# Kernel tuning notes

Measured on AMD Instinct MI355X. Metric: run time of the kernel, lower is better.

## Reference

```python
import jax, jax.numpy as jnp
import numpy as np

NEG_SLOPE = 0.2  # PyG GATConv default leaky_relu slope


def gat_conv(x, src, dst, n, W, a_src, a_dst, bias, concat):
    """PyG-style GATConv (add_self_loops already applied to src/dst)."""
    H, C = a_src.shape
    h = (x @ W).reshape(n, H, C)                      # [N,H,C]
    al_src = jnp.einsum('nhc,hc->nh', h, a_src)       # [N,H]
    al_dst = jnp.einsum('nhc,hc->nh', h, a_dst)       # [N,H]
    e = jax.nn.leaky_relu(al_src[src] + al_dst[dst], NEG_SLOPE)  # [E,H]
    # segment softmax over incoming edges of each dst node
    m = jax.ops.segment_max(e, dst, num_segments=n)   # [N,H]
    ex = jnp.exp(e - m[dst])
    denom = jax.ops.segment_sum(ex, dst, num_segments=n)
    alpha = ex / denom[dst]                            # [E,H]
    out = jax.ops.segment_sum(h[src] * alpha[:, :, None], dst, num_segments=n)  # [N,H,C]
    if concat:
        out = out.reshape(n, H * C)
    else:
        out = out.mean(axis=1)
    return out + bias


def setup_inputs() -> dict:
    key = jax.random.key(0)
    ks = jax.random.split(key, 12)
    N, E = 100000, 1600000
    IN, HID, OUT, H = 128, 16, 32, 4
    x = jax.random.normal(ks[0], (N, IN), dtype=jnp.float32)
    edge_index = jax.random.randint(ks[1], (2, E), 0, N, dtype=jnp.int64)
    s = 0.1
    W1 = jax.random.normal(ks[2], (IN, H * HID), dtype=jnp.float32) * s
    a_src1 = jax.random.normal(ks[3], (H, HID), dtype=jnp.float32) * s
    a_dst1 = jax.random.normal(ks[4], (H, HID), dtype=jnp.float32) * s
    b1 = jnp.zeros((H * HID,), dtype=jnp.float32)
    W2 = jax.random.normal(ks[5], (H * HID, H * OUT), dtype=jnp.float32) * s
    a_src2 = jax.random.normal(ks[6], (H, OUT), dtype=jnp.float32) * s
    a_dst2 = jax.random.normal(ks[7], (H, OUT), dtype=jnp.float32) * s
    b2 = jnp.zeros((OUT,), dtype=jnp.float32)
    return {"x": x, "edge_index": edge_index,
            "W1": W1, "a_src1": a_src1, "a_dst1": a_dst1, "b1": b1,
            "W2": W2, "a_src2": a_src2, "a_dst2": a_dst2, "b2": b2}


def reference(x, edge_index, W1, a_src1, a_dst1, b1, W2, a_src2, a_dst2, b2):
    n = x.shape[0]
    loop = jnp.arange(n, dtype=edge_index.dtype)
    src = jnp.concatenate([edge_index[0], loop])
    dst = jnp.concatenate([edge_index[1], loop])
    # dropout is identity at inference
    h = gat_conv(x, src, dst, n, W1, a_src1, a_dst1, b1, concat=True)
    h = gat_conv(h, src, dst, n, W2, a_src2, a_dst2, b2, concat=False)
    h = jax.nn.elu(h)
    return jax.nn.log_softmax(h, axis=1)
```

## Files before the change

### kernel.cpp

```cpp
#include <hip/hip_runtime.h>
#include <hip/hip_fp16.h>
#include <cstdint>
#include <cstddef>

#define NEG 0.2f
#define TILE 4096
#define WEXP(e) __expf((e) > 0.f ? (e) : NEG * (e))

typedef _Float16 fh2 __attribute__((ext_vector_type(2)));

__device__ __forceinline__ fh2 bfh2(unsigned v) { fh2 r; *(unsigned*)&r = v; return r; }
__device__ __forceinline__ __half2 bch(int v) { __half2 r; *(int*)&r = v; return r; }

#if __has_builtin(__builtin_amdgcn_fdot2)
#define FDOT2(a, b, c) __builtin_amdgcn_fdot2((a), (b), (c), false)
#else
__device__ __forceinline__ float FDOT2(fh2 a, fh2 b, float c) {
    return fmaf((float)a.x, (float)b.x, fmaf((float)a.y, (float)b.y, c));
}
#endif


__global__ __launch_bounds__(256) void bhist_k(const int* __restrict__ ei, int* __restrict__ bc, int E, int nbk) {
    __shared__ int sb[256];
    int t = threadIdx.x;
    sb[t] = 0;
    __syncthreads();
    int stride = gridDim.x * 256;
    for (int i = blockIdx.x * 256 + t; i < E; i += stride) {
        int d = __builtin_nontemporal_load(ei + E + i);
        atomicAdd(&sb[d >> 9], 1);
    }
    __syncthreads();
    if (t < nbk && sb[t] > 0) atomicAdd(&bc[t], sb[t]);
}


__global__ __launch_bounds__(256) void bscan_k(const int* __restrict__ bc, int* __restrict__ bb,
                                               int* __restrict__ curA, int nbk) {
    __shared__ int sm[256];
    int t = threadIdx.x;
    int v = (t < nbk) ? bc[t] : 0;
    sm[t] = v; __syncthreads();
    for (int off = 1; off < 256; off <<= 1) {
        int u = (t >= off) ? sm[t - off] : 0;
        __syncthreads();
        sm[t] += u;
        __syncthreads();
    }
    if (t < nbk) {
        int ex = sm[t] - v;
        bb[t] = ex;
        curA[t] = ex;
        if (t == nbk - 1) bb[nbk] = sm[t];
    }
}


__global__ __launch_bounds__(256) void partA_k(const int* __restrict__ ei, int* __restrict__ curA,
                                               uint2* __restrict__ pairs, int E, int nbk) {
    __shared__ int scnt[256];
    __shared__ int sc[256];
    __shared__ int sbase[256];
    __shared__ int gbase[256];
    __shared__ int cur2[256];
    __shared__ int ssrc[TILE];
    __shared__ int sdst[TILE];
    int t = threadIdx.x;
    int ntiles = (E + TILE - 1) / TILE;
    for (int tile = blockIdx.x; tile < ntiles; tile += gridDim.x) {
        int base = tile * TILE;
        int cntE = min(TILE, E - base);
        scnt[t] = 0;
        __syncthreads();
        int mys[16], myd[16];
        #pragma unroll
        for (int j = 0; j < 16; j++) {
            int i = base + t + 256 * j;
            int s = 0, d = -1;
            if (i < E) {
                s = __builtin_nontemporal_load(ei + i);
                d = __builtin_nontemporal_load(ei + E + i);
            }
            mys[j] = s; myd[j] = d;
            if (d >= 0) atomicAdd(&scnt[d >> 9], 1);
        }
        __syncthreads();
        sc[t] = scnt[t];
        __syncthreads();
        for (int off = 1; off < 256; off <<= 1) {
            int u = (t >= off) ? sc[t - off] : 0;
            __syncthreads();
            sc[t] += u;
            __syncthreads();
        }
        int myb = sc[t] - scnt[t];
        sbase[t] = myb;
        cur2[t] = myb;
        if (t < nbk && scnt[t] > 0) gbase[t] = atomicAdd(&curA[t], scnt[t]);
        __syncthreads();
        #pragma unroll
        for (int j = 0; j < 16; j++) {
            int d = myd[j];
            if (d >= 0) {
                int b = d >> 9;
                int pos = atomicAdd(&cur2[b], 1);
                ssrc[pos] = mys[j];
                sdst[pos] = d;
            }
        }
        __syncthreads();
        for (int i = t; i < cntE; i += 256) {
            int d = sdst[i];
            int b = d >> 9;
            int addr = gbase[b] + (i - sbase[b]);
            pairs[addr] = make_uint2((unsigned)ssrc[i], (unsigned)d);
        }
        __syncthreads();
    }
}


__global__ __launch_bounds__(256) void partB2_k(const uint2* __restrict__ pin, const int* __restrict__ bb,
                                                int* __restrict__ rp, int* __restrict__ cnt,
                                                int* __restrict__ srcout, int N) {
    __shared__ int cur[512];
    __shared__ int sc[512];
    int b = blockIdx.x, t = threadIdx.x;
    int d0 = b << 9;
    cur[t] = 0; cur[t + 256] = 0;
    __syncthreads();
    int ebase = bb[b], eend = bb[b + 1];
    for (int j = ebase + t; j < eend; j += 256) {
        int d = (int)pin[j].y;
        atomicAdd(&cur[d - d0], 1);
    }
    __syncthreads();
    sc[t] = cur[t]; sc[t + 256] = cur[t + 256];
    __syncthreads();
    for (int off = 1; off <= 256; off <<= 1) {
        int a0 = (t >= off) ? sc[t - off] : 0;
        int a1 = sc[t + 256 - off];
        __syncthreads();
        sc[t] += a0; sc[t + 256] += a1;
        __syncthreads();
    }
    int base0 = ebase + sc[t] - cur[t];
    int base1 = ebase + sc[t + 256] - cur[t + 256];
    if (d0 + t < N)       { rp[d0 + t] = base0;       cnt[d0 + t] = cur[t]; }
    if (d0 + t + 256 < N) { rp[d0 + t + 256] = base1; cnt[d0 + t + 256] = cur[t + 256]; }
    cur[t] = base0; cur[t + 256] = base1;
    __syncthreads();
    for (int j = ebase + t; j < eend; j += 256) {
        uint2 p = pin[j];
        int d = (int)p.y;
        int pos = atomicAdd(&cur[d - d0], 1);
        srcout[pos] = (int)p.x;
    }
}


__global__ __launch_bounds__(256) void gemm1_k(const float* __restrict__ x, const float* __restrict__ W,
                                               const float* __restrict__ a_src, const float* __restrict__ a_dst,
                                               __half* __restrict__ h, float* __restrict__ alsrc,
                                               float* __restrict__ aldst, int N) {
    __shared__ float Bs[128 * 64];
    __shared__ float xs[64][68];
    int t = threadIdx.x;
    for (int i = t; i < 128 * 64 / 4; i += 256)
        ((float4*)Bs)[i] = ((const float4*)W)[i];
    int ct = t & 15, rt = t >> 4;
    int head = ct >> 2, cq = ct & 3;
    float asv[4], adv[4];
    #pragma unroll
    for (int j = 0; j < 4; j++) {
        asv[j] = a_src[head * 16 + 4 * cq + j];
        adv[j] = a_dst[head * 16 + 4 * cq + j];
    }
    int ntiles = (N + 63) >> 6;
    for (int tile = blockIdx.x; tile < ntiles; tile += gridDim.x) {
        int r0 = tile << 6;
        float acc[4][4];
        #pragma unroll
        for (int i = 0; i < 4; i++)
            #pragma unroll
            for (int j = 0; j < 4; j++) acc[i][j] = 0.f;
        for (int kc = 0; kc < 128; kc += 64) {
            __syncthreads();
            int srow = t >> 4, sf4 = t & 15;
            #pragma unroll
            for (int p = 0; p < 4; p++) {
                int r = r0 + srow + 16 * p;
                float4 v = make_float4(0.f, 0.f, 0.f, 0.f);
                if (r < N) v = *(const float4*)(x + (size_t)r * 128 + kc + 4 * sf4);
                *(float4*)&xs[srow + 16 * p][4 * sf4] = v;
            }
            __syncthreads();
            #pragma unroll 4
            for (int k = 0; k < 64; k++) {
                float4 bv = *(float4*)&Bs[(kc + k) * 64 + 4 * ct];
                #pragma unroll
                for (int i = 0; i < 4; i++) {
                    float xv = xs[4 * rt + i][k];
                    acc[i][0] = fmaf(xv, bv.x, acc[i][0]);
                    acc[i][1] = fmaf(xv, bv.y, acc[i][1]);
                    acc[i][2] = fmaf(xv, bv.z, acc[i][2]);
                    acc[i][3] = fmaf(xv, bv.w, acc[i][3]);
                }
            }
        }
        #pragma unroll
        for (int i = 0; i < 4; i++) {
            int r = r0 + 4 * rt + i;
            float ps = 0.f, pd = 0.f;
            #pragma unroll
            for (int j = 0; j < 4; j++) {
                ps = fmaf(acc[i][j], asv[j], ps);
                pd = fmaf(acc[i][j], adv[j], pd);
            }
            ps += __shfl_xor(ps, 1); ps += __shfl_xor(ps, 2);
            pd += __shfl_xor(pd, 1); pd += __shfl_xor(pd, 2);
            if (r < N) {
                __half2 h0 = __floats2half2_rn(acc[i][0], acc[i][1]);
                __half2 h1 = __floats2half2_rn(acc[i][2], acc[i][3]);
                *(__half2*)(h + (size_t)r * 64 + 4 * ct) = h0;
                *(__half2*)(h + (size_t)r * 64 + 4 * ct + 2) = h1;
                if (cq == 0) { alsrc[r * 4 + head] = ps; aldst[r * 4 + head] = pd; }
            }
        }
    }
}


__global__ __launch_bounds__(256) void node1_k(const __half* __restrict__ h, const int* __restrict__ srccol,
                                               const float* __restrict__ alsrc, const float* __restrict__ aldst,
                                               const int* __restrict__ rp, const int* __restrict__ cnt,
                                               const float* __restrict__ bias, __half* __restrict__ out, int N) {
    int t = threadIdx.x;
    int d = (blockIdx.x * 256 + t) >> 4;
    if (d >= N) return;
    int c = t & 15;
    int hc = c >> 2;
    const __half2* hb = (const __half2*)h;
    unsigned co = 2u * c;
    float ad = aldst[d * 4 + hc];
    float e = alsrc[d * 4 + hc] + ad;
    float w = WEXP(e);
    float den = w;
    __half2 wp = __float2half2_rn(w);
    uint2 u = *(const uint2*)(hb + ((unsigned)d << 5) + co);
    __half2 acc0 = __hmul2(wp, *(__half2*)&u.x);
    __half2 acc1 = __hmul2(wp, *(__half2*)&u.y);
    int start = rp[d], deg = cnt[d];
    int i = 0;
    for (; i + 3 < deg; i += 4) {
        int s0 = srccol[start + i];
        int s1 = srccol[start + i + 1];
        int s2 = srccol[start + i + 2];
        int s3 = srccol[start + i + 3];
        uint2 u0 = *(const uint2*)(hb + ((unsigned)s0 << 5) + co);
        uint2 u1 = *(const uint2*)(hb + ((unsigned)s1 << 5) + co);
        uint2 u2 = *(const uint2*)(hb + ((unsigned)s2 << 5) + co);
        uint2 u3 = *(const uint2*)(hb + ((unsigned)s3 << 5) + co);
        float e0 = alsrc[s0 * 4 + hc] + ad;
        float e1 = alsrc[s1 * 4 + hc] + ad;
        float e2 = alsrc[s2 * 4 + hc] + ad;
        float e3 = alsrc[s3 * 4 + hc] + ad;
        float w0 = WEXP(e0);
        float w1 = WEXP(e1);
        float w2 = WEXP(e2);
        float w3 = WEXP(e3);
        den += (w0 + w1) + (w2 + w3);
        __half2 p0 = __float2half2_rn(w0), p1 = __float2half2_rn(w1);
        __half2 p2 = __float2half2_rn(w2), p3 = __float2half2_rn(w3);
        acc0 = __hfma2(p0, *(__half2*)&u0.x, acc0);
        acc1 = __hfma2(p0, *(__half2*)&u0.y, acc1);
        acc0 = __hfma2(p1, *(__half2*)&u1.x, acc0);
        acc1 = __hfma2(p1, *(__half2*)&u1.y, acc1);
        acc0 = __hfma2(p2, *(__half2*)&u2.x, acc0);
        acc1 = __hfma2(p2, *(__half2*)&u2.y, acc1);
        acc0 = __hfma2(p3, *(__half2*)&u3.x, acc0);
        acc1 = __hfma2(p3, *(__half2*)&u3.y, acc1);
    }
    for (; i < deg; i++) {
        int s = srccol[start + i];
        uint2 us = *(const uint2*)(hb + ((unsigned)s << 5) + co);
        float es = alsrc[s * 4 + hc] + ad;
        float ws = WEXP(es);
        den += ws;
        __half2 wps = __float2half2_rn(ws);
        acc0 = __hfma2(wps, *(__half2*)&us.x, acc0);
        acc1 = __hfma2(wps, *(__half2*)&us.y, acc1);
    }
    float inv = 1.f / den;
    float2 f0 = __half22float2(acc0), f1 = __half22float2(acc1);
    float4 b = *(const float4*)(bias + 4 * c);
    __half2 o0 = __floats2half2_rn(f0.x * inv + b.x, f0.y * inv + b.y);
    __half2 o1 = __floats2half2_rn(f1.x * inv + b.z, f1.y * inv + b.w);
    uint2 o; o.x = *(unsigned*)&o0; o.y = *(unsigned*)&o1;
    *(uint2*)(out + (size_t)d * 64 + 4 * c) = o;
}


__global__ __launch_bounds__(256) void prew_k(const float* __restrict__ W2, const float* __restrict__ as2,
                                              const float* __restrict__ ad2, float* __restrict__ was,
                                              float* __restrict__ wad) {
    int t = threadIdx.x;
    int k = t >> 2, hh = t & 3;
    const float* wrow = W2 + k * 128 + hh * 32;
    const float* av = as2 + hh * 32;
    const float* dv = ad2 + hh * 32;
    float s = 0.f, ds = 0.f;
    #pragma unroll 8
    for (int c = 0; c < 32; c++) {
        float w = wrow[c];
        s = fmaf(w, av[c], s);
        ds = fmaf(w, dv[c], ds);
    }
    was[t] = s;
    wad[t] = ds;
}


__global__ __launch_bounds__(256) void alv2_k(const __half* __restrict__ h1o, const float* __restrict__ was,
                                              const float* __restrict__ wad, float* __restrict__ alsrc,
                                              float* __restrict__ aldst, int N) {
    int t = threadIdx.x;
    int d = (blockIdx.x * 256 + t) >> 4;
    if (d >= N) return;
    int c = t & 15;
    uint2 u = *(const uint2*)(h1o + (size_t)d * 64 + 4 * c);
    float2 f0 = __half22float2(*(__half2*)&u.x);
    float2 f1 = __half22float2(*(__half2*)&u.y);
    float v0 = f0.x, v1 = f0.y, v2 = f1.x, v3 = f1.y;
    const float4* was4 = (const float4*)was;
    const float4* wad4 = (const float4*)wad;
    float4 wa0 = was4[4 * c + 0], wa1 = was4[4 * c + 1], wa2 = was4[4 * c + 2], wa3 = was4[4 * c + 3];
    float4 wd0 = wad4[4 * c + 0], wd1 = wad4[4 * c + 1], wd2 = wad4[4 * c + 2], wd3 = wad4[4 * c + 3];
    float4 ps, pd;
    ps.x = fmaf(v0, wa0.x, fmaf(v1, wa1.x, fmaf(v2, wa2.x, v3 * wa3.x)));
    ps.y = fmaf(v0, wa0.y, fmaf(v1, wa1.y, fmaf(v2, wa2.y, v3 * wa3.y)));
    ps.z = fmaf(v0, wa0.z, fmaf(v1, wa1.z, fmaf(v2, wa2.z, v3 * wa3.z)));
    ps.w = fmaf(v0, wa0.w, fmaf(v1, wa1.w, fmaf(v2, wa2.w, v3 * wa3.w)));
    pd.x = fmaf(v0, wd0.x, fmaf(v1, wd1.x, fmaf(v2, wd2.x, v3 * wd3.x)));
    pd.y = fmaf(v0, wd0.y, fmaf(v1, wd1.y, fmaf(v2, wd2.y, v3 * wd3.y)));
    pd.z = fmaf(v0, wd0.z, fmaf(v1, wd1.z, fmaf(v2, wd2.z, v3 * wd3.z)));
    pd.w = fmaf(v0, wd0.w, fmaf(v1, wd1.w, fmaf(v2, wd2.w, v3 * wd3.w)));
    #pragma unroll
    for (int off = 1; off <= 8; off <<= 1) {
        ps.x += __shfl_xor(ps.x, off); ps.y += __shfl_xor(ps.y, off);
        ps.z += __shfl_xor(ps.z, off); ps.w += __shfl_xor(ps.w, off);
        pd.x += __shfl_xor(pd.x, off); pd.y += __shfl_xor(pd.y, off);
        pd.z += __shfl_xor(pd.z, off); pd.w += __shfl_xor(pd.w, off);
    }
    if (c == 0) {
        *(float4*)(alsrc + (size_t)d * 4) = ps;
        *(float4*)(aldst + (size_t)d * 4) = pd;
    }
}


#define EDGE_SH(J, U) { \
    __half2 l_ = *(__half2*)&U.x, h_ = *(__half2*)&U.y; \
    __half2 qa = bch(__shfl(wi, 4 * J + 0, 16)); \
    __half2 qb = bch(__shfl(wi, 4 * J + 1, 16)); \
    __half2 qc = bch(__shfl(wi, 4 * J + 2, 16)); \
    __half2 qd = bch(__shfl(wi, 4 * J + 3, 16)); \
    aA0 = __hfma2(qa, l_, aA0); aA1 = __hfma2(qa, h_, aA1); \
    aB0 = __hfma2(qb, l_, aB0); aB1 = __hfma2(qb, h_, aB1); \
    aC0 = __hfma2(qc, l_, aC0); aC1 = __hfma2(qc, h_, aC1); \
    aD0 = __hfma2(qd, l_, aD0); aD1 = __hfma2(qd, h_, aD1); }

__global__ __launch_bounds__(256) void node2_k(const __half* __restrict__ h1o, const int* __restrict__ srccol,
                                               const float* __restrict__ alsrc, const float* __restrict__ aldst,
                                               const int* __restrict__ rp, const int* __restrict__ cnt,
                                               __half* __restrict__ y, int N) {
    int t = threadIdx.x;
    int d = (blockIdx.x * 256 + t) >> 4;
    if (d >= N) return;
    int c = t & 15;
    int eh = c >> 2;
    int hh = c & 3;
    const uint2* hb = (const uint2*)h1o;
    float myad = aldst[d * 4 + hh];
    float selfw = WEXP(alsrc[d * 4 + hh] + myad);
    __half2 selfh = __float2half2_rn(selfw);
    int selfi = *(int*)&selfh;
    float mden = (eh == 0) ? selfw : 0.f;
    uint2 u = hb[((size_t)d << 4) + c];
    __half2 lo = *(__half2*)&u.x, hi = *(__half2*)&u.y;
    __half2 sA = bch(__shfl(selfi, 0, 16));
    __half2 sB = bch(__shfl(selfi, 1, 16));
    __half2 sC = bch(__shfl(selfi, 2, 16));
    __half2 sD = bch(__shfl(selfi, 3, 16));
    __half2 aA0 = __hmul2(sA, lo), aA1 = __hmul2(sA, hi);
    __half2 aB0 = __hmul2(sB, lo), aB1 = __hmul2(sB, hi);
    __half2 aC0 = __hmul2(sC, lo), aC1 = __hmul2(sC, hi);
    __half2 aD0 = __hmul2(sD, lo), aD1 = __hmul2(sD, hi);
    int start = rp[d], deg = cnt[d];
    int i = 0;
    for (; i + 3 < deg; i += 4) {
        int s0 = srccol[start + i];
        int s1 = srccol[start + i + 1];
        int s2 = srccol[start + i + 2];
        int s3 = srccol[start + i + 3];
        uint2 u0 = hb[((size_t)s0 << 4) + c];
        uint2 u1 = hb[((size_t)s1 << 4) + c];
        uint2 u2 = hb[((size_t)s2 << 4) + c];
        uint2 u3 = hb[((size_t)s3 << 4) + c];
        int my = (eh == 0) ? s0 : (eh == 1) ? s1 : (eh == 2) ? s2 : s3;
        float w = WEXP(alsrc[my * 4 + hh] + myad);
        mden += w;
        __half2 wh = __float2half2_rn(w);
        int wi = *(int*)&wh;
        EDGE_SH(0, u0)
        EDGE_SH(1, u1)
        EDGE_SH(2, u2)
        EDGE_SH(3, u3)
    }
    for (; i < deg; i++) {
        int s = srccol[start + i];
        uint2 us = hb[((size_t)s << 4) + c];
        float w = WEXP(alsrc[s * 4 + hh] + myad);
        mden += (eh == 0) ? w : 0.f;
        __half2 wh = __float2half2_rn(w);
        int wi = *(int*)&wh;
        EDGE_SH(0, us)
    }
    mden += __shfl_xor(mden, 4, 16);
    mden += __shfl_xor(mden, 8, 16);
    float dnA = __shfl(mden, 0, 16);
    float dnB = __shfl(mden, 1, 16);
    float dnC = __shfl(mden, 2, 16);
    float dnD = __shfl(mden, 3, 16);
    __half2 jA = __float2half2_rn(0.25f / dnA), jB = __float2half2_rn(0.25f / dnB);
    __half2 jC = __float2half2_rn(0.25f / dnC), jD = __float2half2_rn(0.25f / dnD);
    uint2 oA, oB, oC, oD;
    ((__half2*)&oA)[0] = __hmul2(jA, aA0); ((__half2*)&oA)[1] = __hmul2(jA, aA1);
    ((__half2*)&oB)[0] = __hmul2(jB, aB0); ((__half2*)&oB)[1] = __hmul2(jB, aB1);
    ((__half2*)&oC)[0] = __hmul2(jC, aC0); ((__half2*)&oC)[1] = __hmul2(jC, aC1);
    ((__half2*)&oD)[0] = __hmul2(jD, aD0); ((__half2*)&oD)[1] = __hmul2(jD, aD1);
    __half* yp = y + (size_t)d * 256 + 4u * (unsigned)c;
    *(uint2*)(yp)       = oA;
    *(uint2*)(yp + 64)  = oB;
    *(uint2*)(yp + 128) = oC;
    *(uint2*)(yp + 192) = oD;
}


__global__ __launch_bounds__(256) void gemm3_k(const __half* __restrict__ y, const float* __restrict__ W2,
                                               const float* __restrict__ bias, float* __restrict__ out, int N) {
    __shared__ unsigned wk[128 * 32];
    __shared__ unsigned ys[64 * 130];
    int t = threadIdx.x;
    for (int i = t; i < 4096; i += 256) {
        int k2 = i >> 5, col = i & 31;
        int hh = k2 >> 5, kk = (2 * k2) & 63;
        float f0 = W2[kk * 128 + hh * 32 + col];
        float f1 = W2[(kk + 1) * 128 + hh * 32 + col];
        __half2 hv = __floats2half2_rn(f0, f1);
        wk[i] = *(unsigned*)&hv;
    }
    int ct = t & 7, rt = t >> 3;
    float4 b4 = *(const float4*)(bias + 4 * ct);
    int r0 = blockIdx.x << 6;
    for (int i = t; i < 64 * 64; i += 256) {
        int row = i >> 6, k4 = i & 63;
        uint2 v = make_uint2(0u, 0u);
        int r = r0 + row;
        if (r < N) v = *(const uint2*)(y + (size_t)r * 256 + 4 * k4);
        *(uint2*)&ys[row * 130 + 2 * k4] = v;
    }
    __syncthreads();
    float acc[2][4];
    #pragma unroll
    for (int r = 0; r < 2; r++)
        #pragma unroll
        for (int j = 0; j < 4; j++) acc[r][j] = 0.f;
    const unsigned* yr0 = ys + (2 * rt) * 130;
    const unsigned* yr1 = yr0 + 130;
    const unsigned* wp = wk + 4 * ct;
    #pragma unroll 8
    for (int k2 = 0; k2 < 128; k2++) {
        fh2 xa = bfh2(yr0[k2]);
        fh2 xb = bfh2(yr1[k2]);
        uint2 w01 = *(const uint2*)&wp[k2 * 32];
        uint2 w23 = *(const uint2*)&wp[k2 * 32 + 2];
        fh2 w0 = bfh2(w01.x), w1 = bfh2(w01.y), w2 = bfh2(w23.x), w3 = bfh2(w23.y);
        acc[0][0] = FDOT2(xa, w0, acc[0][0]);
        acc[0][1] = FDOT2(xa, w1, acc[0][1]);
        acc[0][2] = FDOT2(xa, w2, acc[0][2]);
        acc[0][3] = FDOT2(xa, w3, acc[0][3]);
        acc[1][0] = FDOT2(xb, w0, acc[1][0]);
        acc[1][1] = FDOT2(xb, w1, acc[1][1]);
        acc[1][2] = FDOT2(xb, w2, acc[1][2]);
        acc[1][3] = FDOT2(xb, w3, acc[1][3]);
    }
    #pragma unroll
    for (int r = 0; r < 2; r++) {
        int row = r0 + 2 * rt + r;
        float ev0 = acc[r][0] + b4.x;
        float ev1 = acc[r][1] + b4.y;
        float ev2 = acc[r][2] + b4.z;
        float ev3 = acc[r][3] + b4.w;
        ev0 = ev0 > 0.f ? ev0 : __expf(ev0) - 1.f;
        ev1 = ev1 > 0.f ? ev1 : __expf(ev1) - 1.f;
        ev2 = ev2 > 0.f ? ev2 : __expf(ev2) - 1.f;
        ev3 = ev3 > 0.f ? ev3 : __expf(ev3) - 1.f;
        float mx = fmaxf(fmaxf(ev0, ev1), fmaxf(ev2, ev3));
        #pragma unroll
        for (int off = 1; off <= 4; off <<= 1) mx = fmaxf(mx, __shfl_xor(mx, off));
        float sm = __expf(ev0 - mx) + __expf(ev1 - mx) + __expf(ev2 - mx) + __expf(ev3 - mx);
        #pragma unroll
        for (int off = 1; off <= 4; off <<= 1) sm += __shfl_xor(sm, off);
        float ls = mx + __logf(sm);
        if (row < N) {
            float4 o;
            o.x = ev0 - ls; o.y = ev1 - ls; o.z = ev2 - ls; o.w = ev3 - ls;
            *(float4*)(out + (size_t)row * 32 + 4 * ct) = o;
        }
    }
}


extern "C" void kernel_launch(void* const* d_in, const int* in_sizes, int n_in,
                              void* d_out, int out_size, void* d_ws, size_t ws_size,
                              hipStream_t stream) {
    const float* x   = (const float*)d_in[0];
    const int*   ei  = (const int*)d_in[1];
    const float* W1  = (const float*)d_in[2];
    const float* as1 = (const float*)d_in[3];
    const float* ad1 = (const float*)d_in[4];
    const float* b1  = (const float*)d_in[5];
    const float* W2  = (const float*)d_in[6];
    const float* as2 = (const float*)d_in[7];
    const float* ad2 = (const float*)d_in[8];
    const float* b2  = (const float*)d_in[9];
    float* out = (float*)d_out;
    int N = in_sizes[0] / 128;
    int E = in_sizes[1] / 2;

    char* base = (char*)d_ws;
    size_t off = 0;
    auto alloc = [&](size_t bytes) -> char* {
        char* p = base + off;
        off = (off + bytes + 255) & ~(size_t)255;
        return p;
    };
    __half* y     = (__half*)alloc((size_t)N * 256 * 2);
    __half* h1h   = (__half*)y;
    uint2*  pairs = (uint2*)((char*)y + (size_t)N * 64 * 2);
    __half* h1o   = (__half*)alloc((size_t)N * 64 * 2);
    float* alsrc1 = (float*)alloc((size_t)N * 4 * 4);
    float* aldst1 = (float*)alloc((size_t)N * 4 * 4);
    float* alsrc2 = (float*)alloc((size_t)N * 4 * 4);
    float* aldst2 = (float*)alloc((size_t)N * 4 * 4);
    float* was    = (float*)alloc(256 * 4);
    float* wad    = (float*)alloc(256 * 4);
    int* cnt  = (int*)alloc((size_t)N * 4);
    int* rp   = (int*)alloc((size_t)N * 4);
    int* curA = (int*)alloc(256 * 4);
    int* bc   = (int*)alloc(256 * 4);
    int* bb   = (int*)alloc(260 * 4);
    int* srccol = (int*)alloc((size_t)E * 4);

    int nbk = (N + 511) >> 9;
    int ntilesA = (E + TILE - 1) / TILE;
    int nt1 = (N + 63) >> 6;

    prew_k<<<1, 256, 0, stream>>>(W2, as2, ad2, was, wad);
    hipMemsetAsync(bc, 0, 256 * 4, stream);
    bhist_k<<<512, 256, 0, stream>>>(ei, bc, E, nbk);
    bscan_k<<<1, 256, 0, stream>>>(bc, bb, curA, nbk);
    partA_k<<<ntilesA, 256, 0, stream>>>(ei, curA, pairs, E, nbk);
    partB2_k<<<nbk, 256, 0, stream>>>(pairs, bb, rp, cnt, srccol, N);

    gemm1_k<<<(nt1 + 1) / 2, 256, 0, stream>>>(x, W1, as1, ad1, h1h, alsrc1, aldst1, N);
    node1_k<<<(N + 15) / 16, 256, 0, stream>>>(h1h, srccol, alsrc1, aldst1, rp, cnt, b1, h1o, N);
    alv2_k<<<(N + 15) / 16, 256, 0, stream>>>(h1o, was, wad, alsrc2, aldst2, N);
    node2_k<<<(N + 15) / 16, 256, 0, stream>>>(h1o, srccol, alsrc2, aldst2, rp, cnt, y, N);
    gemm3_k<<<nt1, 256, 0, stream>>>(y, W2, b2, out, N);
}
```

Measured before the change: 344.0 us.

## Fuse layer-2 attention logits into node1, prefetch edge gathers, retile gemm3

Merges the alv2 pass into node1, so layer-2 attention logits come from the freshly computed node output without a second kernel reading h1o. Both aggregation kernels now load source indices as 16-byte vectors. They also software-pipeline the gathers one quad ahead and share one attention exp per lane through shuffles. gemm3 moves to 32-row tiles with packed fp16 FMA accumulation flushed to fp32 every 16 k-steps, instead of fdot2 into fp32, which adds precision risk in exchange for throughput.

```diff
diff --git a/kernel.cpp b/kernel.cpp
--- a/kernel.cpp
+++ b/kernel.cpp
@@ -7,18 +7,15 @@
 #define TILE 4096
 #define WEXP(e) __expf((e) > 0.f ? (e) : NEG * (e))
 
-typedef _Float16 fh2 __attribute__((ext_vector_type(2)));
-
-__device__ __forceinline__ fh2 bfh2(unsigned v) { fh2 r; *(unsigned*)&r = v; return r; }
-__device__ __forceinline__ __half2 bch(int v) { __half2 r; *(int*)&r = v; return r; }
-
-#if __has_builtin(__builtin_amdgcn_fdot2)
-#define FDOT2(a, b, c) __builtin_amdgcn_fdot2((a), (b), (c), false)
-#else
-__device__ __forceinline__ float FDOT2(fh2 a, fh2 b, float c) {
-    return fmaf((float)a.x, (float)b.x, fmaf((float)a.y, (float)b.y, c));
-}
-#endif
+typedef int i4v __attribute__((ext_vector_type(4)));
+
+__device__ __forceinline__ i4v ld_i4(const int* p) {
+    i4v r;
+    __builtin_memcpy(&r, p, 16);
+    return r;
+}
+__device__ __forceinline__ __half2 bch(unsigned v) { __half2 r; *(unsigned*)&r = v; return r; }
+__device__ __forceinline__ __half2 bchi(int v) { __half2 r; *(int*)&r = v; return r; }
 
 
 __global__ __launch_bounds__(256) void bhist_k(const int* __restrict__ ei, int* __restrict__ bc, int E, int nbk) {
@@ -232,76 +229,6 @@
 }
 
 
-__global__ __launch_bounds__(256) void node1_k(const __half* __restrict__ h, const int* __restrict__ srccol,
-                                               const float* __restrict__ alsrc, const float* __restrict__ aldst,
-                                               const int* __restrict__ rp, const int* __restrict__ cnt,
-                                               const float* __restrict__ bias, __half* __restrict__ out, int N) {
-    int t = threadIdx.x;
-    int d = (blockIdx.x * 256 + t) >> 4;
-    if (d >= N) return;
-    int c = t & 15;
-    int hc = c >> 2;
-    const __half2* hb = (const __half2*)h;
-    unsigned co = 2u * c;
-    float ad = aldst[d * 4 + hc];
-    float e = alsrc[d * 4 + hc] + ad;
-    float w = WEXP(e);
-    float den = w;
-    __half2 wp = __float2half2_rn(w);
-    uint2 u = *(const uint2*)(hb + ((unsigned)d << 5) + co);
-    __half2 acc0 = __hmul2(wp, *(__half2*)&u.x);
-    __half2 acc1 = __hmul2(wp, *(__half2*)&u.y);
-    int start = rp[d], deg = cnt[d];
-    int i = 0;
-    for (; i + 3 < deg; i += 4) {
-        int s0 = srccol[start + i];
-        int s1 = srccol[start + i + 1];
-        int s2 = srccol[start + i + 2];
-        int s3 = srccol[start + i + 3];
-        uint2 u0 = *(const uint2*)(hb + ((unsigned)s0 << 5) + co);
-        uint2 u1 = *(const uint2*)(hb + ((unsigned)s1 << 5) + co);
-        uint2 u2 = *(const uint2*)(hb + ((unsigned)s2 << 5) + co);
-        uint2 u3 = *(const uint2*)(hb + ((unsigned)s3 << 5) + co);
-        float e0 = alsrc[s0 * 4 + hc] + ad;
-        float e1 = alsrc[s1 * 4 + hc] + ad;
-        float e2 = alsrc[s2 * 4 + hc] + ad;
-        float e3 = alsrc[s3 * 4 + hc] + ad;
-        float w0 = WEXP(e0);
-        float w1 = WEXP(e1);
-        float w2 = WEXP(e2);
-        float w3 = WEXP(e3);
-        den += (w0 + w1) + (w2 + w3);
-        __half2 p0 = __float2half2_rn(w0), p1 = __float2half2_rn(w1);
-        __half2 p2 = __float2half2_rn(w2), p3 = __float2half2_rn(w3);
-        acc0 = __hfma2(p0, *(__half2*)&u0.x, acc0);
-        acc1 = __hfma2(p0, *(__half2*)&u0.y, acc1);
-        acc0 = __hfma2(p1, *(__half2*)&u1.x, acc0);
-        acc1 = __hfma2(p1, *(__half2*)&u1.y, acc1);
-        acc0 = __hfma2(p2, *(__half2*)&u2.x, acc0);
-        acc1 = __hfma2(p2, *(__half2*)&u2.y, acc1);
-        acc0 = __hfma2(p3, *(__half2*)&u3.x, acc0);
-        acc1 = __hfma2(p3, *(__half2*)&u3.y, acc1);
-    }
-    for (; i < deg; i++) {
-        int s = srccol[start + i];
-        uint2 us = *(const uint2*)(hb + ((unsigned)s << 5) + co);
-        float es = alsrc[s * 4 + hc] + ad;
-        float ws = WEXP(es);
-        den += ws;
-        __half2 wps = __float2half2_rn(ws);
-        acc0 = __hfma2(wps, *(__half2*)&us.x, acc0);
-        acc1 = __hfma2(wps, *(__half2*)&us.y, acc1);
-    }
-    float inv = 1.f / den;
-    float2 f0 = __half22float2(acc0), f1 = __half22float2(acc1);
-    float4 b = *(const float4*)(bias + 4 * c);
-    __half2 o0 = __floats2half2_rn(f0.x * inv + b.x, f0.y * inv + b.y);
-    __half2 o1 = __floats2half2_rn(f1.x * inv + b.z, f1.y * inv + b.w);
-    uint2 o; o.x = *(unsigned*)&o0; o.y = *(unsigned*)&o1;
-    *(uint2*)(out + (size_t)d * 64 + 4 * c) = o;
-}
-
-
 __global__ __launch_bounds__(256) void prew_k(const float* __restrict__ W2, const float* __restrict__ as2,
                                               const float* __restrict__ ad2, float* __restrict__ was,
                                               float* __restrict__ wad) {
@@ -322,17 +249,91 @@
 }
 
 
-__global__ __launch_bounds__(256) void alv2_k(const __half* __restrict__ h1o, const float* __restrict__ was,
-                                              const float* __restrict__ wad, float* __restrict__ alsrc,
-                                              float* __restrict__ aldst, int N) {
+__global__ __launch_bounds__(256) void node1_k(const __half* __restrict__ h, const int* __restrict__ srccol,
+                                               const float* __restrict__ alsrc, const float* __restrict__ aldst,
+                                               const int* __restrict__ rp, const int* __restrict__ cnt,
+                                               const float* __restrict__ bias,
+                                               const float* __restrict__ was, const float* __restrict__ wad,
+                                               __half* __restrict__ out,
+                                               float* __restrict__ alsrc2, float* __restrict__ aldst2, int N) {
     int t = threadIdx.x;
     int d = (blockIdx.x * 256 + t) >> 4;
     if (d >= N) return;
     int c = t & 15;
-    uint2 u = *(const uint2*)(h1o + (size_t)d * 64 + 4 * c);
-    float2 f0 = __half22float2(*(__half2*)&u.x);
-    float2 f1 = __half22float2(*(__half2*)&u.y);
-    float v0 = f0.x, v1 = f0.y, v2 = f1.x, v3 = f1.y;
+    int eh = c >> 2, hh = c & 3;
+    int mh = c >> 2;
+    const uint2* hb = (const uint2*)h;
+    float myad = aldst[d * 4 + hh];
+    float selfw = WEXP(alsrc[d * 4 + hh] + myad);
+    __half2 sh2 = __float2half2_rn(selfw);
+    int si = *(int*)&sh2;
+    float mden = (eh == 0) ? selfw : 0.f;
+    uint2 u = hb[((size_t)d << 4) + c];
+    __half2 smy = bchi(__shfl(si, mh, 16));
+    __half2 acc0 = __hmul2(smy, bch(u.x));
+    __half2 acc1 = __hmul2(smy, bch(u.y));
+    int start = rp[d], deg = cnt[d];
+    int nq = deg >> 2;
+    int i = 0;
+    #define N1_PROC(G0, G1, G2, G3, AW) { \
+        float w_ = WEXP((AW) + myad); \
+        mden += w_; \
+        __half2 wh_ = __float2half2_rn(w_); \
+        int wi_ = *(int*)&wh_; \
+        __half2 q0_ = bchi(__shfl(wi_, 0 + mh, 16)); \
+        __half2 q1_ = bchi(__shfl(wi_, 4 + mh, 16)); \
+        __half2 q2_ = bchi(__shfl(wi_, 8 + mh, 16)); \
+        __half2 q3_ = bchi(__shfl(wi_, 12 + mh, 16)); \
+        acc0 = __hfma2(q0_, bch(G0.x), acc0); acc1 = __hfma2(q0_, bch(G0.y), acc1); \
+        acc0 = __hfma2(q1_, bch(G1.x), acc0); acc1 = __hfma2(q1_, bch(G1.y), acc1); \
+        acc0 = __hfma2(q2_, bch(G2.x), acc0); acc1 = __hfma2(q2_, bch(G2.y), acc1); \
+        acc0 = __hfma2(q3_, bch(G3.x), acc0); acc1 = __hfma2(q3_, bch(G3.y), acc1); }
+    if (nq > 0) {
+        i4v sv = ld_i4(srccol + start);
+        uint2 g0 = hb[((size_t)(unsigned)sv.x << 4) + c];
+        uint2 g1 = hb[((size_t)(unsigned)sv.y << 4) + c];
+        uint2 g2 = hb[((size_t)(unsigned)sv.z << 4) + c];
+        uint2 g3 = hb[((size_t)(unsigned)sv.w << 4) + c];
+        int my = (eh == 0) ? sv.x : (eh == 1) ? sv.y : (eh == 2) ? sv.z : sv.w;
+        float aw = alsrc[(size_t)my * 4 + hh];
+        i4v nv = (nq > 1) ? ld_i4(srccol + start + 4) : sv;
+        for (int q = 1; q < nq; q++) {
+            uint2 n0 = hb[((size_t)(unsigned)nv.x << 4) + c];
+            uint2 n1 = hb[((size_t)(unsigned)nv.y << 4) + c];
+            uint2 n2 = hb[((size_t)(unsigned)nv.z << 4) + c];
+            uint2 n3 = hb[((size_t)(unsigned)nv.w << 4) + c];
+            int nmy = (eh == 0) ? nv.x : (eh == 1) ? nv.y : (eh == 2) ? nv.z : nv.w;
+            float naw = alsrc[(size_t)nmy * 4 + hh];
+            i4v nv2 = (q + 1 < nq) ? ld_i4(srccol + start + 4 * (q + 1)) : nv;
+            N1_PROC(g0, g1, g2, g3, aw)
+            g0 = n0; g1 = n1; g2 = n2; g3 = n3; aw = naw; nv = nv2;
+        }
+        N1_PROC(g0, g1, g2, g3, aw)
+        i = nq << 2;
+    }
+    for (; i < deg; i++) {
+        int s = srccol[start + i];
+        uint2 us = hb[((size_t)(unsigned)s << 4) + c];
+        float w = WEXP(alsrc[(size_t)s * 4 + hh] + myad);
+        mden += (eh == 0) ? w : 0.f;
+        __half2 wh = __float2half2_rn(w);
+        int wi = *(int*)&wh;
+        __half2 qq = bchi(__shfl(wi, mh, 16));
+        acc0 = __hfma2(qq, bch(us.x), acc0);
+        acc1 = __hfma2(qq, bch(us.y), acc1);
+    }
+    mden += __shfl_xor(mden, 4, 16);
+    mden += __shfl_xor(mden, 8, 16);
+    float den = __shfl(mden, mh, 16);
+    float inv = 1.f / den;
+    float2 f0 = __half22float2(acc0), f1 = __half22float2(acc1);
+    float4 b = *(const float4*)(bias + 4 * c);
+    float v0 = f0.x * inv + b.x, v1 = f0.y * inv + b.y;
+    float v2 = f1.x * inv + b.z, v3 = f1.y * inv + b.w;
+    __half2 o0 = __floats2half2_rn(v0, v1);
+    __half2 o1 = __floats2half2_rn(v2, v3);
+    uint2 o; o.x = *(unsigned*)&o0; o.y = *(unsigned*)&o1;
+    *(uint2*)(out + (size_t)d * 64 + 4 * c) = o;
     const float4* was4 = (const float4*)was;
     const float4* wad4 = (const float4*)wad;
     float4 wa0 = was4[4 * c + 0], wa1 = was4[4 * c + 1], wa2 = was4[4 * c + 2], wa3 = was4[4 * c + 3];
@@ -354,18 +355,18 @@
         pd.z += __shfl_xor(pd.z, off); pd.w += __shfl_xor(pd.w, off);
     }
     if (c == 0) {
-        *(float4*)(alsrc + (size_t)d * 4) = ps;
-        *(float4*)(aldst + (size_t)d * 4) = pd;
+        *(float4*)(alsrc2 + (size_t)d * 4) = ps;
+        *(float4*)(aldst2 + (size_t)d * 4) = pd;
     }
 }
 
 
 #define EDGE_SH(J, U) { \
-    __half2 l_ = *(__half2*)&U.x, h_ = *(__half2*)&U.y; \
-    __half2 qa = bch(__shfl(wi, 4 * J + 0, 16)); \
-    __half2 qb = bch(__shfl(wi, 4 * J + 1, 16)); \
-    __half2 qc = bch(__shfl(wi, 4 * J + 2, 16)); \
-    __half2 qd = bch(__shfl(wi, 4 * J + 3, 16)); \
+    __half2 l_ = bch(U.x), h_ = bch(U.y); \
+    __half2 qa = bchi(__shfl(wi, 4 * J + 0, 16)); \
+    __half2 qb = bchi(__shfl(wi, 4 * J + 1, 16)); \
+    __half2 qc = bchi(__shfl(wi, 4 * J + 2, 16)); \
+    __half2 qd = bchi(__shfl(wi, 4 * J + 3, 16)); \
     aA0 = __hfma2(qa, l_, aA0); aA1 = __hfma2(qa, h_, aA1); \
     aB0 = __hfma2(qb, l_, aB0); aB1 = __hfma2(qb, h_, aB1); \
     aC0 = __hfma2(qc, l_, aC0); aC1 = __hfma2(qc, h_, aC1); \
@@ -388,40 +389,51 @@
     int selfi = *(int*)&selfh;
     float mden = (eh == 0) ? selfw : 0.f;
     uint2 u = hb[((size_t)d << 4) + c];
-    __half2 lo = *(__half2*)&u.x, hi = *(__half2*)&u.y;
-    __half2 sA = bch(__shfl(selfi, 0, 16));
-    __half2 sB = bch(__shfl(selfi, 1, 16));
-    __half2 sC = bch(__shfl(selfi, 2, 16));
-    __half2 sD = bch(__shfl(selfi, 3, 16));
+    __half2 lo = bch(u.x), hi = bch(u.y);
+    __half2 sA = bchi(__shfl(selfi, 0, 16));
+    __half2 sB = bchi(__shfl(selfi, 1, 16));
+    __half2 sC = bchi(__shfl(selfi, 2, 16));
+    __half2 sD = bchi(__shfl(selfi, 3, 16));
     __half2 aA0 = __hmul2(sA, lo), aA1 = __hmul2(sA, hi);
     __half2 aB0 = __hmul2(sB, lo), aB1 = __hmul2(sB, hi);
     __half2 aC0 = __hmul2(sC, lo), aC1 = __hmul2(sC, hi);
     __half2 aD0 = __hmul2(sD, lo), aD1 = __hmul2(sD, hi);
     int start = rp[d], deg = cnt[d];
+    int nq = deg >> 2;
     int i = 0;
-    for (; i + 3 < deg; i += 4) {
-        int s0 = srccol[start + i];
-        int s1 = srccol[start + i + 1];
-        int s2 = srccol[start + i + 2];
-        int s3 = srccol[start + i + 3];
-        uint2 u0 = hb[((size_t)s0 << 4) + c];
-        uint2 u1 = hb[((size_t)s1 << 4) + c];
-        uint2 u2 = hb[((size_t)s2 << 4) + c];
-        uint2 u3 = hb[((size_t)s3 << 4) + c];
-        int my = (eh == 0) ? s0 : (eh == 1) ? s1 : (eh == 2) ? s2 : s3;
-        float w = WEXP(alsrc[my * 4 + hh] + myad);
-        mden += w;
-        __half2 wh = __float2half2_rn(w);
-        int wi = *(int*)&wh;
-        EDGE_SH(0, u0)
-        EDGE_SH(1, u1)
-        EDGE_SH(2, u2)
-        EDGE_SH(3, u3)
+    #define N2_PROC(G0, G1, G2, G3, AW) { \
+        float w_ = WEXP((AW) + myad); \
+        mden += w_; \
+        __half2 wh_ = __float2half2_rn(w_); \
+        int wi = *(int*)&wh_; \
+        EDGE_SH(0, G0) EDGE_SH(1, G1) EDGE_SH(2, G2) EDGE_SH(3, G3) }
+    if (nq > 0) {
+        i4v sv = ld_i4(srccol + start);
+        uint2 g0 = hb[((size_t)(unsigned)sv.x << 4) + c];
+        uint2 g1 = hb[((size_t)(unsigned)sv.y << 4) + c];
+        uint2 g2 = hb[((size_t)(unsigned)sv.z << 4) + c];
+        uint2 g3 = hb[((size_t)(unsigned)sv.w << 4) + c];
+        int my = (eh == 0) ? sv.x : (eh == 1) ? sv.y : (eh == 2) ? sv.z : sv.w;
+        float aw = alsrc[(size_t)my * 4 + hh];
+        i4v nv = (nq > 1) ? ld_i4(srccol + start + 4) : sv;
+        for (int q = 1; q < nq; q++) {
+            uint2 n0 = hb[((size_t)(unsigned)nv.x << 4) + c];
+            uint2 n1 = hb[((size_t)(unsigned)nv.y << 4) + c];
+            uint2 n2 = hb[((size_t)(unsigned)nv.z << 4) + c];
+            uint2 n3 = hb[((size_t)(unsigned)nv.w << 4) + c];
+            int nmy = (eh == 0) ? nv.x : (eh == 1) ? nv.y : (eh == 2) ? nv.z : nv.w;
+            float naw = alsrc[(size_t)nmy * 4 + hh];
+            i4v nv2 = (q + 1 < nq) ? ld_i4(srccol + start + 4 * (q + 1)) : nv;
+            N2_PROC(g0, g1, g2, g3, aw)
+            g0 = n0; g1 = n1; g2 = n2; g3 = n3; aw = naw; nv = nv2;
+        }
+        N2_PROC(g0, g1, g2, g3, aw)
+        i = nq << 2;
     }
     for (; i < deg; i++) {
         int s = srccol[start + i];
-        uint2 us = hb[((size_t)s << 4) + c];
-        float w = WEXP(alsrc[s * 4 + hh] + myad);
+        uint2 us = hb[((size_t)(unsigned)s << 4) + c];
+        float w = WEXP(alsrc[(size_t)s * 4 + hh] + myad);
         mden += (eh == 0) ? w : 0.f;
         __half2 wh = __float2half2_rn(w);
         int wi = *(int*)&wh;
@@ -451,7 +463,7 @@
 __global__ __launch_bounds__(256) void gemm3_k(const __half* __restrict__ y, const float* __restrict__ W2,
                                                const float* __restrict__ bias, float* __restrict__ out, int N) {
     __shared__ unsigned wk[128 * 32];
-    __shared__ unsigned ys[64 * 130];
+    __shared__ unsigned ys[32 * 130];
     int t = threadIdx.x;
     for (int i = t; i < 4096; i += 256) {
         int k2 = i >> 5, col = i & 31;
@@ -463,8 +475,8 @@
     }
     int ct = t & 7, rt = t >> 3;
     float4 b4 = *(const float4*)(bias + 4 * ct);
-    int r0 = blockIdx.x << 6;
-    for (int i = t; i < 64 * 64; i += 256) {
+    int r0 = blockIdx.x << 5;
+    for (int i = t; i < 32 * 64; i += 256) {
         int row = i >> 6, k4 = i & 63;
         uint2 v = make_uint2(0u, 0u);
         int r = r0 + row;
@@ -472,53 +484,49 @@
         *(uint2*)&ys[row * 130 + 2 * k4] = v;
     }
     __syncthreads();
-    float acc[2][4];
+    float acc[4] = {0.f, 0.f, 0.f, 0.f};
+    const unsigned* yr = ys + rt * 130;
+    const unsigned* wp = wk + 4 * ct;
+    for (int kc = 0; kc < 128; kc += 16) {
+        __half2 h0 = __float2half2_rn(0.f), h1 = h0, h2 = h0, h3 = h0;
+        #pragma unroll
+        for (int j = 0; j < 16; j++) {
+            int k2 = kc + j;
+            __half2 x2 = bch(yr[k2]);
+            uint2 w01 = *(const uint2*)&wp[k2 * 32];
+            uint2 w23 = *(const uint2*)&wp[k2 * 32 + 2];
+            h0 = __hfma2(x2, bch(w01.x), h0);
+            h1 = __hfma2(x2, bch(w01.y), h1);
+            h2 = __hfma2(x2, bch(w23.x), h2);
+            h3 = __hfma2(x2, bch(w23.y), h3);
+        }
+        float2 q0 = __half22float2(h0), q1 = __half22float2(h1);
+        float2 q2 = __half22float2(h2), q3 = __half22float2(h3);
+        acc[0] += q0.x + q0.y;
+        acc[1] += q1.x + q1.y;
+        acc[2] += q2.x + q2.y;
+        acc[3] += q3.x + q3.y;
+    }
+    int row = r0 + rt;
+    float ev0 = acc[0] + b4.x;
+    float ev1 = acc[1] + b4.y;
+    float ev2 = acc[2] + b4.z;
+    float ev3 = acc[3] + b4.w;
+    ev0 = ev0 > 0.f ? ev0 : __expf(ev0) - 1.f;
+    ev1 = ev1 > 0.f ? ev1 : __expf(ev1) - 1.f;
+    ev2 = ev2 > 0.f ? ev2 : __expf(ev2) - 1.f;
+    ev3 = ev3 > 0.f ? ev3 : __expf(ev3) - 1.f;
+    float mx = fmaxf(fmaxf(ev0, ev1), fmaxf(ev2, ev3));
     #pragma unroll
-    for (int r = 0; r < 2; r++)
-        #pragma unroll
-        for (int j = 0; j < 4; j++) acc[r][j] = 0.f;
-    const unsigned* yr0 = ys + (2 * rt) * 130;
-    const unsigned* yr1 = yr0 + 130;
-    const unsigned* wp = wk + 4 * ct;
-    #pragma unroll 8
-    for (int k2 = 0; k2 < 128; k2++) {
-        fh2 xa = bfh2(yr0[k2]);
-        fh2 xb = bfh2(yr1[k2]);
-        uint2 w01 = *(const uint2*)&wp[k2 * 32];
-        uint2 w23 = *(const uint2*)&wp[k2 * 32 + 2];
-        fh2 w0 = bfh2(w01.x), w1 = bfh2(w01.y), w2 = bfh2(w23.x), w3 = bfh2(w23.y);
-        acc[0][0] = FDOT2(xa, w0, acc[0][0]);
-        acc[0][1] = FDOT2(xa, w1, acc[0][1]);
-        acc[0][2] = FDOT2(xa, w2, acc[0][2]);
-        acc[0][3] = FDOT2(xa, w3, acc[0][3]);
-        acc[1][0] = FDOT2(xb, w0, acc[1][0]);
-        acc[1][1] = FDOT2(xb, w1, acc[1][1]);
-        acc[1][2] = FDOT2(xb, w2, acc[1][2]);
-        acc[1][3] = FDOT2(xb, w3, acc[1][3]);
-    }
+    for (int off = 1; off <= 4; off <<= 1) mx = fmaxf(mx, __shfl_xor(mx, off));
+    float sm = __expf(ev0 - mx) + __expf(ev1 - mx) + __expf(ev2 - mx) + __expf(ev3 - mx);
     #pragma unroll
-    for (int r = 0; r < 2; r++) {
-        int row = r0 + 2 * rt + r;
-        float ev0 = acc[r][0] + b4.x;
-        float ev1 = acc[r][1] + b4.y;
-        float ev2 = acc[r][2] + b4.z;
-        float ev3 = acc[r][3] + b4.w;
-        ev0 = ev0 > 0.f ? ev0 : __expf(ev0) - 1.f;
-        ev1 = ev1 > 0.f ? ev1 : __expf(ev1) - 1.f;
-        ev2 = ev2 > 0.f ? ev2 : __expf(ev2) - 1.f;
-        ev3 = ev3 > 0.f ? ev3 : __expf(ev3) - 1.f;
-        float mx = fmaxf(fmaxf(ev0, ev1), fmaxf(ev2, ev3));
-        #pragma unroll
-        for (int off = 1; off <= 4; off <<= 1) mx = fmaxf(mx, __shfl_xor(mx, off));
-        float sm = __expf(ev0 - mx) + __expf(ev1 - mx) + __expf(ev2 - mx) + __expf(ev3 - mx);
-        #pragma unroll
-        for (int off = 1; off <= 4; off <<= 1) sm += __shfl_xor(sm, off);
-        float ls = mx + __logf(sm);
-        if (row < N) {
-            float4 o;
-            o.x = ev0 - ls; o.y = ev1 - ls; o.z = ev2 - ls; o.w = ev3 - ls;
-            *(float4*)(out + (size_t)row * 32 + 4 * ct) = o;
-        }
+    for (int off = 1; off <= 4; off <<= 1) sm += __shfl_xor(sm, off);
+    float ls = mx + __logf(sm);
+    if (row < N) {
+        float4 o;
+        o.x = ev0 - ls; o.y = ev1 - ls; o.z = ev2 - ls; o.w = ev3 - ls;
+        *(float4*)(out + (size_t)row * 32 + 4 * ct) = o;
     }
 }
 
@@ -567,6 +575,7 @@
     int nbk = (N + 511) >> 9;
     int ntilesA = (E + TILE - 1) / TILE;
     int nt1 = (N + 63) >> 6;
+    int nt3 = (N + 31) >> 5;
 
     prew_k<<<1, 256, 0, stream>>>(W2, as2, ad2, was, wad);
     hipMemsetAsync(bc, 0, 256 * 4, stream);
@@ -576,8 +585,8 @@
     partB2_k<<<nbk, 256, 0, stream>>>(pairs, bb, rp, cnt, srccol, N);
 
     gemm1_k<<<(nt1 + 1) / 2, 256, 0, stream>>>(x, W1, as1, ad1, h1h, alsrc1, aldst1, N);
-    node1_k<<<(N + 15) / 16, 256, 0, stream>>>(h1h, srccol, alsrc1, aldst1, rp, cnt, b1, h1o, N);
-    alv2_k<<<(N + 15) / 16, 256, 0, stream>>>(h1o, was, wad, alsrc2, aldst2, N);
+    node1_k<<<(N + 15) / 16, 256, 0, stream>>>(h1h, srccol, alsrc1, aldst1, rp, cnt, b1,
+                                               was, wad, h1o, alsrc2, aldst2, N);
     node2_k<<<(N + 15) / 16, 256, 0, stream>>>(h1o, srccol, alsrc2, aldst2, rp, cnt, y, N);
-    gemm3_k<<<nt1, 256, 0, stream>>>(y, W2, b2, out, N);
-}
+    gemm3_k<<<nt3, 256, 0, stream>>>(y, W2, b2, out, N);
+}
```

Result: faster. 333.1 us (-3.2%).
